# Performance work log

Measured on AMD Instinct MI355X. Metric: run time of the kernel, lower is better.

Reference implementation:

```python
import jax, jax.numpy as jnp
import numpy as np

BLOCK = 8
ITERS = 8
EPS = 1e-5
SHAPE = (64, 64, 64)
BATCH = 16


def overlapping_blocks(x, bs):
    # x: [B, M, N, K] -> per-block copies with a 1-cell zero-padded halo:
    # [B, nm, nn, nk, bs+2, bs+2, bs+2]
    B, M, N, K = x.shape
    p = jnp.pad(x, ((0, 0), (1, 1), (1, 1), (1, 1)))

    def gather(a, axis, n, size):
        idx = (jnp.arange(n)[:, None] * bs + jnp.arange(size)[None, :]).reshape(-1)
        a = jnp.take(a, idx, axis=axis)
        return a.reshape(a.shape[:axis] + (n, size) + a.shape[axis + 1:])

    nm, nn, nk = M // bs, N // bs, K // bs
    p = gather(p, 1, nm, bs + 2)   # [B, nm, P, N+2, K+2]
    p = gather(p, 3, nn, bs + 2)   # [B, nm, P, nn, P, K+2]
    p = gather(p, 5, nk, bs + 2)   # [B, nm, P, nn, P, nk, P]
    return p.transpose(0, 1, 3, 5, 2, 4, 6)


def param_blocks(w, bs):
    # [..., M, N, K] -> [..., nm, nn, nk, bs, bs, bs] (non-overlapping)
    lead = w.shape[:-3]
    M, N, K = w.shape[-3:]
    w = w.reshape(*lead, M // bs, bs, N // bs, bs, K // bs, bs)
    nl = len(lead)
    perm = tuple(range(nl)) + (nl, nl + 2, nl + 4, nl + 1, nl + 3, nl + 5)
    return w.transpose(perm)


def gridnet_step(weight, bias, residual_scale, x, inner_iterations, block_size,
                 eps=EPS, normalize=True):
    bs = block_size
    blocks = overlapping_blocks(x, bs)            # [B, nm, nn, nk, P, P, P]
    wb = param_blocks(weight, bs)                 # [27, nm, nn, nk, bs, bs, bs]
    bb = param_blocks(bias, bs)                   # [nm, nn, nk, bs, bs, bs]
    rb = param_blocks(residual_scale, bs)
    inner = (slice(None),) * 4 + (slice(1, -1),) * 3

    for _ in range(inner_iterations):
        if normalize:
            mean = blocks.mean(axis=(-3, -2, -1), keepdims=True)
            var = blocks.var(axis=(-3, -2, -1), keepdims=True)
            normed = (blocks - mean) / jnp.sqrt(var + eps)
        else:
            normed = blocks
        dot = jnp.zeros_like(blocks[inner])
        tap = 0
        for dx in range(3):
            for dy in range(3):
                for dz in range(3):
                    nb = normed[..., dx:dx + bs, dy:dy + bs, dz:dz + bs]
                    dot = dot + nb * wb[tap]
                    tap += 1
        out = blocks[inner] + rb * jax.nn.silu(dot + bb)
        # only interior cells update; halo stays at initial (synced) values
        blocks = blocks.at[inner].set(out)

    y = blocks[inner]                              # [B, nm, nn, nk, bs, bs, bs]
    B, nm, nn, nk = y.shape[:4]
    return y.transpose(0, 1, 4, 2, 5, 3, 6).reshape(B, nm * bs, nn * bs, nk * bs)


def setup_inputs() -> dict:
    key = jax.random.key(0)
    k_w, k_x = jax.random.split(key)
    M, N, K = SHAPE
    weight = jax.random.normal(k_w, (27, M, N, K), dtype=jnp.float32) / np.sqrt(27.0).astype(np.float32)
    bias = jnp.zeros((M, N, K), dtype=jnp.float32)
    residual_scale = jnp.ones((M, N, K), dtype=jnp.float32)
    x = jax.random.normal(k_x, (BATCH, M, N, K), dtype=jnp.float32)
    return {"weight": weight, "bias": bias, "residual_scale": residual_scale, "x": x}


def reference(weight, bias, residual_scale, x):
    return gridnet_step(weight, bias, residual_scale, x, ITERS, BLOCK, EPS, True)
```

## Files before the change

kernel.cpp:

```cpp
#include <hip/hip_runtime.h>

typedef _Float16 h2 __attribute__((ext_vector_type(2)));
typedef _Float16 h8 __attribute__((ext_vector_type(8)));

#define WSTRIDE 108

template <int CTRL>
__device__ __forceinline__ float dpp_stage(float v) {
    int x = __builtin_amdgcn_update_dpp(0, __float_as_int(v), CTRL, 0xf, 0xf, true);
    return v + __int_as_float(x);
}
__device__ __forceinline__ float wave_sum(float v) {
    v = dpp_stage<0x111>(v);
    v = dpp_stage<0x112>(v);
    v = dpp_stage<0x114>(v);
    v = dpp_stage<0x118>(v);
    v = dpp_stage<0x142>(v);
    v = dpp_stage<0x143>(v);
    return v;
}
__device__ __forceinline__ float bcast63(float v) {
    return __int_as_float(__builtin_amdgcn_readlane(__float_as_int(v), 63));
}
__device__ __forceinline__ h2 mid2(h2 lo, h2 hi) {
    int r = __builtin_amdgcn_alignbit(__builtin_bit_cast(int, hi),
                                      __builtin_bit_cast(int, lo), 16);
    return __builtin_bit_cast(h2, r);
}
__device__ __forceinline__ h2 pkrtz(float a, float b) {
    return __builtin_bit_cast(h2, __builtin_amdgcn_cvt_pkrtz(a, b));
}

#define MEMFENCE() asm volatile("" ::: "memory")

#define SL(W, K) __builtin_shufflevector(W, W, 2*(K), 2*(K)+1)

#define COLT(O, T) {                                                           \
    h8 WA = wp8[(T)];                                                          \
    h8 WB = wp8[(T) + 1];                                                      \
    h8 WC = wp8[(T) + 2];                                                      \
    h2 D0 = bp[(O) + 0], D1 = bp[(O) + 1], D2 = bp[(O) + 2],                   \
       D3 = bp[(O) + 3], D4 = bp[(O) + 4];                                     \
    h2 M0 = mid2(D0, D1), M1 = mid2(D1, D2), M2 = mid2(D2, D3),                \
       M3 = mid2(D3, D4);                                                      \
    dd0 = __builtin_elementwise_fma(D0, SL(WA, 0), dd0);                       \
    dd1 = __builtin_elementwise_fma(D1, SL(WA, 1), dd1);                       \
    dd2 = __builtin_elementwise_fma(D2, SL(WA, 2), dd2);                       \
    dd3 = __builtin_elementwise_fma(D3, SL(WA, 3), dd3);                       \
    dd0 = __builtin_elementwise_fma(M0, SL(WB, 0), dd0);                       \
    dd1 = __builtin_elementwise_fma(M1, SL(WB, 1), dd1);                       \
    dd2 = __builtin_elementwise_fma(M2, SL(WB, 2), dd2);                       \
    dd3 = __builtin_elementwise_fma(M3, SL(WB, 3), dd3);                       \
    dd0 = __builtin_elementwise_fma(D1, SL(WC, 0), dd0);                       \
    dd1 = __builtin_elementwise_fma(D2, SL(WC, 1), dd1);                       \
    dd2 = __builtin_elementwise_fma(D3, SL(WC, 2), dd2);                       \
    dd3 = __builtin_elementwise_fma(D4, SL(WC, 3), dd3); }

#define OUTK(CK, DDF, SWK, BK, RK) {                                           \
    float u = fmaf(fmaf(SWK, nmean, DDF), istd, BK);                           \
    CK += RK * (u * __builtin_amdgcn_rcpf(1.f + __expf(-u))); }

__global__ __launch_bounds__(512, 1)
void gridnet_kernel(const float* __restrict__ W,
                    const float* __restrict__ Bias,
                    const float* __restrict__ Rs,
                    const float* __restrict__ X,
                    float* __restrict__ Y,
                    int n_batch)
{
    __shared__ __align__(16) int wlds[64 * WSTRIDE];
    __shared__ __align__(16) h2 dbuf[8][500];

    const int tid  = threadIdx.x;
    const int wave = tid >> 6;
    const int lane = tid & 63;
    const int lx   = lane >> 3;
    const int ly   = lane & 7;

    const int no    = n_batch >> 3;
    const int bid   = (int)blockIdx.x;
    const int r     = bid / no;
    const int ob    = bid - r * no;
    const int batch = 8 * ob + wave;
    const int gm0 = (r >> 6) << 3;
    const int gn0 = ((r >> 3) & 7) << 3;
    const int gk0 = (r & 7) << 3;

    const float* xb = X + ((size_t)batch << 18);
    h2* const my = dbuf[wave];

    float s_all = 0.f, q_all = 0.f, s_int = 0.f, q_int = 0.f;
    #pragma unroll 1
    for (int c = lane; c < 100; c += 64) {
        int x = c / 10, y = c - (c / 10) * 10;
        int m = gm0 + x - 1, n = gn0 + y - 1;
        bool row_ok = ((unsigned)m < 64u) & ((unsigned)n < 64u);
        float4 fa = {0.f, 0.f, 0.f, 0.f}, fb = {0.f, 0.f, 0.f, 0.f};
        float vz0 = 0.f, vz9 = 0.f;
        if (row_ok) {
            const float* rp = xb + (m * 4096 + n * 64);
            fa = *(const float4*)(rp + gk0);
            fb = *(const float4*)(rp + gk0 + 4);
            if (gk0 > 0)  vz0 = rp[gk0 - 1];
            if (gk0 < 56) vz9 = rp[gk0 + 8];
        }
        h2 d0 = pkrtz(vz0, fa.x), d1 = pkrtz(fa.y, fa.z), d2 = pkrtz(fa.w, fb.x),
           d3 = pkrtz(fb.y, fb.z), d4 = pkrtz(fb.w, vz9);
        my[c * 5 + 0] = d0; my[c * 5 + 1] = d1; my[c * 5 + 2] = d2;
        my[c * 5 + 3] = d3; my[c * 5 + 4] = d4;
        float t0 = (float)d0.x, t1 = (float)d0.y, t2 = (float)d1.x,
              t3 = (float)d1.y, t4 = (float)d2.x, t5 = (float)d2.y,
              t6 = (float)d3.x, t7 = (float)d3.y, t8 = (float)d4.x,
              t9 = (float)d4.y;
        float s8 = t1 + t2 + t3 + t4 + t5 + t6 + t7 + t8;
        float q8 = t1*t1 + t2*t2 + t3*t3 + t4*t4 + t5*t5 + t6*t6 + t7*t7 + t8*t8;
        s_all += s8 + t0 + t9;
        q_all += q8 + t0*t0 + t9*t9;
        bool inter = ((unsigned)(x - 1) < 8u) & ((unsigned)(y - 1) < 8u);
        if (inter) { s_int += s8; q_int += q8; }
    }

    #pragma unroll 1
    for (int j = tid; j < 1728; j += 512) {
        int tap = j >> 6;
        int pos = j & 63;
        int plx = pos >> 3, ply = pos & 7;
        const float* wp = W + ((size_t)tap << 18)
                        + (((size_t)(gm0 + plx)) << 12) + ((gn0 + ply) << 6) + gk0;
        float4 fa = *(const float4*)(wp);
        float4 fb = *(const float4*)(wp + 4);
        int4 v = { __builtin_bit_cast(int, pkrtz(fa.x, fa.y)),
                   __builtin_bit_cast(int, pkrtz(fa.z, fa.w)),
                   __builtin_bit_cast(int, pkrtz(fb.x, fb.y)),
                   __builtin_bit_cast(int, pkrtz(fb.z, fb.w)) };
        *(int4*)&wlds[pos * WSTRIDE + tap * 4] = v;
    }

    float S_all = bcast63(wave_sum(s_all));
    float Q_all = bcast63(wave_sum(q_all));
    float Si    = bcast63(wave_sum(s_int));
    float Qi    = bcast63(wave_sum(q_int));
    const float halo_s = S_all - Si;
    const float halo_q = Q_all - Qi;

    __syncthreads();

    const h8* const wp8 = (const h8*)&wlds[lane * WSTRIDE];
    h2* const bp = &my[5 * (lx * 10 + ly)];

    float sw0=0.f, sw1=0.f, sw2=0.f, sw3=0.f, sw4=0.f, sw5=0.f, sw6=0.f, sw7=0.f;
    #pragma unroll
    for (int t = 0; t < 27; ++t) {
        h8 w = wp8[t];
        sw0 += (float)w[0]; sw1 += (float)w[1]; sw2 += (float)w[2];
        sw3 += (float)w[3]; sw4 += (float)w[4]; sw5 += (float)w[5];
        sw6 += (float)w[6]; sw7 += (float)w[7];
    }

    const size_t ofs = (((size_t)(gm0 + lx)) << 12) + ((gn0 + ly) << 6) + gk0;
    float4 ba = *(const float4*)(Bias + ofs), bb = *(const float4*)(Bias + ofs + 4);
    float4 ra = *(const float4*)(Rs + ofs),   rb = *(const float4*)(Rs + ofs + 4);

    h2 e0 = bp[55], e1 = bp[56], e2 = bp[57], e3 = bp[58], e4 = bp[59];
    float z0f = (float)e0.x, z9f = (float)e4.y;
    float c1 = (float)e0.y, c2 = (float)e1.x, c3 = (float)e1.y, c4 = (float)e2.x,
          c5 = (float)e2.y, c6 = (float)e3.x, c7 = (float)e3.y, c8 = (float)e4.x;

    const float inv_n = 1.0f / 1000.0f;

    #pragma unroll 1
    for (int it = 0; it < 8; ++it) {
        float mean  = (halo_s + Si) * inv_n;
        float qmean = (halo_q + Qi) * inv_n;
        float istd  = rsqrtf(qmean - mean * mean + 1e-5f);
        float nmean = -mean;

        h2 dd0 = { (_Float16)0.f, (_Float16)0.f };
        h2 dd1 = dd0, dd2 = dd0, dd3 = dd0;
        COLT(0,    0)
        COLT(5,    3)
        COLT(10,   6)
        COLT(50,   9)
        COLT(55,  12)
        COLT(60,  15)
        COLT(100, 18)
        COLT(105, 21)
        COLT(110, 24)

        MEMFENCE();

        OUTK(c1, (float)dd0.x, sw0, ba.x, ra.x)
        OUTK(c2, (float)dd0.y, sw1, ba.y, ra.y)
        OUTK(c3, (float)dd1.x, sw2, ba.z, ra.z)
        OUTK(c4, (float)dd1.y, sw3, ba.w, ra.w)
        OUTK(c5, (float)dd2.x, sw4, bb.x, rb.x)
        OUTK(c6, (float)dd2.y, sw5, bb.y, rb.y)
        OUTK(c7, (float)dd3.x, sw6, bb.z, rb.z)
        OUTK(c8, (float)dd3.y, sw7, bb.w, rb.w)

        if (it != 7) {
            e0 = pkrtz(z0f, c1); e1 = pkrtz(c2, c3); e2 = pkrtz(c4, c5);
            e3 = pkrtz(c6, c7); e4 = pkrtz(c8, z9f);
            bp[55] = e0; bp[56] = e1; bp[57] = e2; bp[58] = e3; bp[59] = e4;

            MEMFENCE();

            float sp = ((c1 + c2) + (c3 + c4)) + ((c5 + c6) + (c7 + c8));
            float qp = ((c1*c1 + c2*c2) + (c3*c3 + c4*c4)) +
                       ((c5*c5 + c6*c6) + (c7*c7 + c8*c8));
            Si = bcast63(wave_sum(sp));
            Qi = bcast63(wave_sum(qp));
        }
    }

    float* yp = Y + ((size_t)batch << 18) + ofs;
    *(float4*)(yp)     = make_float4(c1, c2, c3, c4);
    *(float4*)(yp + 4) = make_float4(c5, c6, c7, c8);
}

extern "C" void kernel_launch(void* const* d_in, const int* in_sizes, int n_in,
                              void* d_out, int out_size, void* d_ws, size_t ws_size,
                              hipStream_t stream) {
    const float* W = (const float*)d_in[0];
    const float* B = (const float*)d_in[1];
    const float* R = (const float*)d_in[2];
    const float* X = (const float*)d_in[3];
    float* Y = (float*)d_out;

    int n_batch = in_sizes[3] >> 18;
    dim3 grid(512 * (n_batch >> 3)), block(512);
    hipLaunchKernelGGL(gridnet_kernel, grid, block, 0, stream, W, B, R, X, Y, n_batch);
}
```

Baseline: 147.0 us.

## Process two batch elements per wave to reuse stencil weights from registers

Each wave now handles two batch samples, so the block shrinks from 8 waves to 4 while still covering 8 samples. Every weight vector read from LDS feeds the FMAs of both samples, which halves weight LDS traffic per output and gives more independent FMA chains for instruction-level parallelism. The cost is roughly doubled register pressure and fewer waves per block, which can cut latency hiding and occupancy.

```diff
diff --git a/kernel.cpp b/kernel.cpp
--- a/kernel.cpp
+++ b/kernel.cpp
@@ -35,32 +35,48 @@
 
 #define SL(W, K) __builtin_shufflevector(W, W, 2*(K), 2*(K)+1)
 
-#define COLT(O, T) {                                                           \
+#define COLT2(O, T) {                                                          \
     h8 WA = wp8[(T)];                                                          \
     h8 WB = wp8[(T) + 1];                                                      \
     h8 WC = wp8[(T) + 2];                                                      \
-    h2 D0 = bp[(O) + 0], D1 = bp[(O) + 1], D2 = bp[(O) + 2],                   \
-       D3 = bp[(O) + 3], D4 = bp[(O) + 4];                                     \
-    h2 M0 = mid2(D0, D1), M1 = mid2(D1, D2), M2 = mid2(D2, D3),                \
-       M3 = mid2(D3, D4);                                                      \
-    dd0 = __builtin_elementwise_fma(D0, SL(WA, 0), dd0);                       \
-    dd1 = __builtin_elementwise_fma(D1, SL(WA, 1), dd1);                       \
-    dd2 = __builtin_elementwise_fma(D2, SL(WA, 2), dd2);                       \
-    dd3 = __builtin_elementwise_fma(D3, SL(WA, 3), dd3);                       \
-    dd0 = __builtin_elementwise_fma(M0, SL(WB, 0), dd0);                       \
-    dd1 = __builtin_elementwise_fma(M1, SL(WB, 1), dd1);                       \
-    dd2 = __builtin_elementwise_fma(M2, SL(WB, 2), dd2);                       \
-    dd3 = __builtin_elementwise_fma(M3, SL(WB, 3), dd3);                       \
-    dd0 = __builtin_elementwise_fma(D1, SL(WC, 0), dd0);                       \
-    dd1 = __builtin_elementwise_fma(D2, SL(WC, 1), dd1);                       \
-    dd2 = __builtin_elementwise_fma(D3, SL(WC, 2), dd2);                       \
-    dd3 = __builtin_elementwise_fma(D4, SL(WC, 3), dd3); }
-
-#define OUTK(CK, DDF, SWK, BK, RK) {                                           \
-    float u = fmaf(fmaf(SWK, nmean, DDF), istd, BK);                           \
+    h2 A0 = bpA[(O) + 0], A1 = bpA[(O) + 1], A2 = bpA[(O) + 2],                \
+       A3 = bpA[(O) + 3], A4 = bpA[(O) + 4];                                   \
+    h2 MA0 = mid2(A0, A1), MA1 = mid2(A1, A2), MA2 = mid2(A2, A3),             \
+       MA3 = mid2(A3, A4);                                                     \
+    h2 B0 = bpB[(O) + 0], B1 = bpB[(O) + 1], B2 = bpB[(O) + 2],                \
+       B3 = bpB[(O) + 3], B4 = bpB[(O) + 4];                                   \
+    h2 MB0 = mid2(B0, B1), MB1 = mid2(B1, B2), MB2 = mid2(B2, B3),             \
+       MB3 = mid2(B3, B4);                                                     \
+    ddA0 = __builtin_elementwise_fma(A0, SL(WA, 0), ddA0);                     \
+    ddA1 = __builtin_elementwise_fma(A1, SL(WA, 1), ddA1);                     \
+    ddA2 = __builtin_elementwise_fma(A2, SL(WA, 2), ddA2);                     \
+    ddA3 = __builtin_elementwise_fma(A3, SL(WA, 3), ddA3);                     \
+    ddB0 = __builtin_elementwise_fma(B0, SL(WA, 0), ddB0);                     \
+    ddB1 = __builtin_elementwise_fma(B1, SL(WA, 1), ddB1);                     \
+    ddB2 = __builtin_elementwise_fma(B2, SL(WA, 2), ddB2);                     \
+    ddB3 = __builtin_elementwise_fma(B3, SL(WA, 3), ddB3);                     \
+    ddA0 = __builtin_elementwise_fma(MA0, SL(WB, 0), ddA0);                    \
+    ddA1 = __builtin_elementwise_fma(MA1, SL(WB, 1), ddA1);                    \
+    ddA2 = __builtin_elementwise_fma(MA2, SL(WB, 2), ddA2);                    \
+    ddA3 = __builtin_elementwise_fma(MA3, SL(WB, 3), ddA3);                    \
+    ddB0 = __builtin_elementwise_fma(MB0, SL(WB, 0), ddB0);                    \
+    ddB1 = __builtin_elementwise_fma(MB1, SL(WB, 1), ddB1);                    \
+    ddB2 = __builtin_elementwise_fma(MB2, SL(WB, 2), ddB2);                    \
+    ddB3 = __builtin_elementwise_fma(MB3, SL(WB, 3), ddB3);                    \
+    ddA0 = __builtin_elementwise_fma(A1, SL(WC, 0), ddA0);                     \
+    ddA1 = __builtin_elementwise_fma(A2, SL(WC, 1), ddA1);                     \
+    ddA2 = __builtin_elementwise_fma(A3, SL(WC, 2), ddA2);                     \
+    ddA3 = __builtin_elementwise_fma(A4, SL(WC, 3), ddA3);                     \
+    ddB0 = __builtin_elementwise_fma(B1, SL(WC, 0), ddB0);                     \
+    ddB1 = __builtin_elementwise_fma(B2, SL(WC, 1), ddB1);                     \
+    ddB2 = __builtin_elementwise_fma(B3, SL(WC, 2), ddB2);                     \
+    ddB3 = __builtin_elementwise_fma(B4, SL(WC, 3), ddB3); }
+
+#define OUTK(CK, DDF, SWK, BK, RK, NM, IS) {                                   \
+    float u = fmaf(fmaf(SWK, NM, DDF), IS, BK);                                \
     CK += RK * (u * __builtin_amdgcn_rcpf(1.f + __expf(-u))); }
 
-__global__ __launch_bounds__(512, 1)
+__global__ __launch_bounds__(256, 1)
 void gridnet_kernel(const float* __restrict__ W,
                     const float* __restrict__ Bias,
                     const float* __restrict__ Rs,
@@ -81,47 +97,64 @@
     const int bid   = (int)blockIdx.x;
     const int r     = bid / no;
     const int ob    = bid - r * no;
-    const int batch = 8 * ob + wave;
+    const int batchA = 8 * ob + 2 * wave;
     const int gm0 = (r >> 6) << 3;
     const int gn0 = ((r >> 3) & 7) << 3;
     const int gk0 = (r & 7) << 3;
 
-    const float* xb = X + ((size_t)batch << 18);
-    h2* const my = dbuf[wave];
-
-    float s_all = 0.f, q_all = 0.f, s_int = 0.f, q_int = 0.f;
+    const float* xb = X + ((size_t)batchA << 18);
+    h2* const myA = dbuf[2 * wave];
+    h2* const myB = dbuf[2 * wave + 1];
+
+    float sA_all = 0.f, qA_all = 0.f, sA_int = 0.f, qA_int = 0.f;
+    float sB_all = 0.f, qB_all = 0.f, sB_int = 0.f, qB_int = 0.f;
     #pragma unroll 1
     for (int c = lane; c < 100; c += 64) {
         int x = c / 10, y = c - (c / 10) * 10;
         int m = gm0 + x - 1, n = gn0 + y - 1;
         bool row_ok = ((unsigned)m < 64u) & ((unsigned)n < 64u);
         float4 fa = {0.f, 0.f, 0.f, 0.f}, fb = {0.f, 0.f, 0.f, 0.f};
-        float vz0 = 0.f, vz9 = 0.f;
+        float4 ga = {0.f, 0.f, 0.f, 0.f}, gb = {0.f, 0.f, 0.f, 0.f};
+        float vz0A = 0.f, vz9A = 0.f, vz0B = 0.f, vz9B = 0.f;
         if (row_ok) {
             const float* rp = xb + (m * 4096 + n * 64);
+            const float* rq = rp + (1 << 18);
             fa = *(const float4*)(rp + gk0);
             fb = *(const float4*)(rp + gk0 + 4);
-            if (gk0 > 0)  vz0 = rp[gk0 - 1];
-            if (gk0 < 56) vz9 = rp[gk0 + 8];
+            ga = *(const float4*)(rq + gk0);
+            gb = *(const float4*)(rq + gk0 + 4);
+            if (gk0 > 0)  { vz0A = rp[gk0 - 1]; vz0B = rq[gk0 - 1]; }
+            if (gk0 < 56) { vz9A = rp[gk0 + 8]; vz9B = rq[gk0 + 8]; }
         }
-        h2 d0 = pkrtz(vz0, fa.x), d1 = pkrtz(fa.y, fa.z), d2 = pkrtz(fa.w, fb.x),
-           d3 = pkrtz(fb.y, fb.z), d4 = pkrtz(fb.w, vz9);
-        my[c * 5 + 0] = d0; my[c * 5 + 1] = d1; my[c * 5 + 2] = d2;
-        my[c * 5 + 3] = d3; my[c * 5 + 4] = d4;
-        float t0 = (float)d0.x, t1 = (float)d0.y, t2 = (float)d1.x,
-              t3 = (float)d1.y, t4 = (float)d2.x, t5 = (float)d2.y,
-              t6 = (float)d3.x, t7 = (float)d3.y, t8 = (float)d4.x,
-              t9 = (float)d4.y;
-        float s8 = t1 + t2 + t3 + t4 + t5 + t6 + t7 + t8;
-        float q8 = t1*t1 + t2*t2 + t3*t3 + t4*t4 + t5*t5 + t6*t6 + t7*t7 + t8*t8;
-        s_all += s8 + t0 + t9;
-        q_all += q8 + t0*t0 + t9*t9;
+        h2 a0 = pkrtz(vz0A, fa.x), a1 = pkrtz(fa.y, fa.z), a2 = pkrtz(fa.w, fb.x),
+           a3 = pkrtz(fb.y, fb.z), a4 = pkrtz(fb.w, vz9A);
+        h2 b0 = pkrtz(vz0B, ga.x), b1 = pkrtz(ga.y, ga.z), b2 = pkrtz(ga.w, gb.x),
+           b3 = pkrtz(gb.y, gb.z), b4 = pkrtz(gb.w, vz9B);
+        myA[c * 5 + 0] = a0; myA[c * 5 + 1] = a1; myA[c * 5 + 2] = a2;
+        myA[c * 5 + 3] = a3; myA[c * 5 + 4] = a4;
+        myB[c * 5 + 0] = b0; myB[c * 5 + 1] = b1; myB[c * 5 + 2] = b2;
+        myB[c * 5 + 3] = b3; myB[c * 5 + 4] = b4;
+        float tA0=(float)a0.x, tA1=(float)a0.y, tA2=(float)a1.x, tA3=(float)a1.y,
+              tA4=(float)a2.x, tA5=(float)a2.y, tA6=(float)a3.x, tA7=(float)a3.y,
+              tA8=(float)a4.x, tA9=(float)a4.y;
+        float tB0=(float)b0.x, tB1=(float)b0.y, tB2=(float)b1.x, tB3=(float)b1.y,
+              tB4=(float)b2.x, tB5=(float)b2.y, tB6=(float)b3.x, tB7=(float)b3.y,
+              tB8=(float)b4.x, tB9=(float)b4.y;
+        float sA8 = tA1+tA2+tA3+tA4+tA5+tA6+tA7+tA8;
+        float qA8 = tA1*tA1+tA2*tA2+tA3*tA3+tA4*tA4+tA5*tA5+tA6*tA6+tA7*tA7+tA8*tA8;
+        float sB8 = tB1+tB2+tB3+tB4+tB5+tB6+tB7+tB8;
+        float qB8 = tB1*tB1+tB2*tB2+tB3*tB3+tB4*tB4+tB5*tB5+tB6*tB6+tB7*tB7+tB8*tB8;
+        sA_all += sA8 + tA0 + tA9;
+        qA_all += qA8 + tA0*tA0 + tA9*tA9;
+        sB_all += sB8 + tB0 + tB9;
+        qB_all += qB8 + tB0*tB0 + tB9*tB9;
         bool inter = ((unsigned)(x - 1) < 8u) & ((unsigned)(y - 1) < 8u);
-        if (inter) { s_int += s8; q_int += q8; }
+        if (inter) { sA_int += sA8; qA_int += qA8;
+                     sB_int += sB8; qB_int += qB8; }
     }
 
     #pragma unroll 1
-    for (int j = tid; j < 1728; j += 512) {
+    for (int j = tid; j < 1728; j += 256) {
         int tap = j >> 6;
         int pos = j & 63;
         int plx = pos >> 3, ply = pos & 7;
@@ -136,17 +169,22 @@
         *(int4*)&wlds[pos * WSTRIDE + tap * 4] = v;
     }
 
-    float S_all = bcast63(wave_sum(s_all));
-    float Q_all = bcast63(wave_sum(q_all));
-    float Si    = bcast63(wave_sum(s_int));
-    float Qi    = bcast63(wave_sum(q_int));
-    const float halo_s = S_all - Si;
-    const float halo_q = Q_all - Qi;
+    float SA_all = bcast63(wave_sum(sA_all));
+    float QA_all = bcast63(wave_sum(qA_all));
+    float SiA    = bcast63(wave_sum(sA_int));
+    float QiA    = bcast63(wave_sum(qA_int));
+    float SB_all = bcast63(wave_sum(sB_all));
+    float QB_all = bcast63(wave_sum(qB_all));
+    float SiB    = bcast63(wave_sum(sB_int));
+    float QiB    = bcast63(wave_sum(qB_int));
+    const float halo_sA = SA_all - SiA, halo_qA = QA_all - QiA;
+    const float halo_sB = SB_all - SiB, halo_qB = QB_all - QiB;
 
     __syncthreads();
 
     const h8* const wp8 = (const h8*)&wlds[lane * WSTRIDE];
-    h2* const bp = &my[5 * (lx * 10 + ly)];
+    h2* const bpA = &myA[5 * (lx * 10 + ly)];
+    h2* const bpB = &myB[5 * (lx * 10 + ly)];
 
     float sw0=0.f, sw1=0.f, sw2=0.f, sw3=0.f, sw4=0.f, sw5=0.f, sw6=0.f, sw7=0.f;
     #pragma unroll
@@ -161,61 +199,87 @@
     float4 ba = *(const float4*)(Bias + ofs), bb = *(const float4*)(Bias + ofs + 4);
     float4 ra = *(const float4*)(Rs + ofs),   rb = *(const float4*)(Rs + ofs + 4);
 
-    h2 e0 = bp[55], e1 = bp[56], e2 = bp[57], e3 = bp[58], e4 = bp[59];
-    float z0f = (float)e0.x, z9f = (float)e4.y;
-    float c1 = (float)e0.y, c2 = (float)e1.x, c3 = (float)e1.y, c4 = (float)e2.x,
-          c5 = (float)e2.y, c6 = (float)e3.x, c7 = (float)e3.y, c8 = (float)e4.x;
+    h2 eA0 = bpA[55], eA1 = bpA[56], eA2 = bpA[57], eA3 = bpA[58], eA4 = bpA[59];
+    h2 eB0 = bpB[55], eB1 = bpB[56], eB2 = bpB[57], eB3 = bpB[58], eB4 = bpB[59];
+    float z0A = (float)eA0.x, z9A = (float)eA4.y;
+    float z0B = (float)eB0.x, z9B = (float)eB4.y;
+    float cA1=(float)eA0.y, cA2=(float)eA1.x, cA3=(float)eA1.y, cA4=(float)eA2.x,
+          cA5=(float)eA2.y, cA6=(float)eA3.x, cA7=(float)eA3.y, cA8=(float)eA4.x;
+    float cB1=(float)eB0.y, cB2=(float)eB1.x, cB3=(float)eB1.y, cB4=(float)eB2.x,
+          cB5=(float)eB2.y, cB6=(float)eB3.x, cB7=(float)eB3.y, cB8=(float)eB4.x;
 
     const float inv_n = 1.0f / 1000.0f;
 
     #pragma unroll 1
     for (int it = 0; it < 8; ++it) {
-        float mean  = (halo_s + Si) * inv_n;
-        float qmean = (halo_q + Qi) * inv_n;
-        float istd  = rsqrtf(qmean - mean * mean + 1e-5f);
-        float nmean = -mean;
-
-        h2 dd0 = { (_Float16)0.f, (_Float16)0.f };
-        h2 dd1 = dd0, dd2 = dd0, dd3 = dd0;
-        COLT(0,    0)
-        COLT(5,    3)
-        COLT(10,   6)
-        COLT(50,   9)
-        COLT(55,  12)
-        COLT(60,  15)
-        COLT(100, 18)
-        COLT(105, 21)
-        COLT(110, 24)
+        float meanA  = (halo_sA + SiA) * inv_n;
+        float istdA  = rsqrtf((halo_qA + QiA) * inv_n - meanA * meanA + 1e-5f);
+        float nmeanA = -meanA;
+        float meanB  = (halo_sB + SiB) * inv_n;
+        float istdB  = rsqrtf((halo_qB + QiB) * inv_n - meanB * meanB + 1e-5f);
+        float nmeanB = -meanB;
+
+        h2 ddA0 = { (_Float16)0.f, (_Float16)0.f };
+        h2 ddA1 = ddA0, ddA2 = ddA0, ddA3 = ddA0;
+        h2 ddB0 = ddA0, ddB1 = ddA0, ddB2 = ddA0, ddB3 = ddA0;
+        COLT2(0,    0)
+        COLT2(5,    3)
+        COLT2(10,   6)
+        COLT2(50,   9)
+        COLT2(55,  12)
+        COLT2(60,  15)
+        COLT2(100, 18)
+        COLT2(105, 21)
+        COLT2(110, 24)
 
         MEMFENCE();
 
-        OUTK(c1, (float)dd0.x, sw0, ba.x, ra.x)
-        OUTK(c2, (float)dd0.y, sw1, ba.y, ra.y)
-        OUTK(c3, (float)dd1.x, sw2, ba.z, ra.z)
-        OUTK(c4, (float)dd1.y, sw3, ba.w, ra.w)
-        OUTK(c5, (float)dd2.x, sw4, bb.x, rb.x)
-        OUTK(c6, (float)dd2.y, sw5, bb.y, rb.y)
-        OUTK(c7, (float)dd3.x, sw6, bb.z, rb.z)
-        OUTK(c8, (float)dd3.y, sw7, bb.w, rb.w)
+        OUTK(cA1, (float)ddA0.x, sw0, ba.x, ra.x, nmeanA, istdA)
+        OUTK(cA2, (float)ddA0.y, sw1, ba.y, ra.y, nmeanA, istdA)
+        OUTK(cA3, (float)ddA1.x, sw2, ba.z, ra.z, nmeanA, istdA)
+        OUTK(cA4, (float)ddA1.y, sw3, ba.w, ra.w, nmeanA, istdA)
+        OUTK(cA5, (float)ddA2.x, sw4, bb.x, rb.x, nmeanA, istdA)
+        OUTK(cA6, (float)ddA2.y, sw5, bb.y, rb.y, nmeanA, istdA)
+        OUTK(cA7, (float)ddA3.x, sw6, bb.z, rb.z, nmeanA, istdA)
+        OUTK(cA8, (float)ddA3.y, sw7, bb.w, rb.w, nmeanA, istdA)
+        OUTK(cB1, (float)ddB0.x, sw0, ba.x, ra.x, nmeanB, istdB)
+        OUTK(cB2, (float)ddB0.y, sw1, ba.y, ra.y, nmeanB, istdB)
+        OUTK(cB3, (float)ddB1.x, sw2, ba.z, ra.z, nmeanB, istdB)
+        OUTK(cB4, (float)ddB1.y, sw3, ba.w, ra.w, nmeanB, istdB)
+        OUTK(cB5, (float)ddB2.x, sw4, bb.x, rb.x, nmeanB, istdB)
+        OUTK(cB6, (float)ddB2.y, sw5, bb.y, rb.y, nmeanB, istdB)
+        OUTK(cB7, (float)ddB3.x, sw6, bb.z, rb.z, nmeanB, istdB)
+        OUTK(cB8, (float)ddB3.y, sw7, bb.w, rb.w, nmeanB, istdB)
 
         if (it != 7) {
-            e0 = pkrtz(z0f, c1); e1 = pkrtz(c2, c3); e2 = pkrtz(c4, c5);
-            e3 = pkrtz(c6, c7); e4 = pkrtz(c8, z9f);
-            bp[55] = e0; bp[56] = e1; bp[57] = e2; bp[58] = e3; bp[59] = e4;
+            eA0 = pkrtz(z0A, cA1); eA1 = pkrtz(cA2, cA3); eA2 = pkrtz(cA4, cA5);
+            eA3 = pkrtz(cA6, cA7); eA4 = pkrtz(cA8, z9A);
+            bpA[55] = eA0; bpA[56] = eA1; bpA[57] = eA2; bpA[58] = eA3; bpA[59] = eA4;
+            eB0 = pkrtz(z0B, cB1); eB1 = pkrtz(cB2, cB3); eB2 = pkrtz(cB4, cB5);
+            eB3 = pkrtz(cB6, cB7); eB4 = pkrtz(cB8, z9B);
+            bpB[55] = eB0; bpB[56] = eB1; bpB[57] = eB2; bpB[58] = eB3; bpB[59] = eB4;
 
             MEMFENCE();
 
-            float sp = ((c1 + c2) + (c3 + c4)) + ((c5 + c6) + (c7 + c8));
-            float qp = ((c1*c1 + c2*c2) + (c3*c3 + c4*c4)) +
-                       ((c5*c5 + c6*c6) + (c7*c7 + c8*c8));
-            Si = bcast63(wave_sum(sp));
-            Qi = bcast63(wave_sum(qp));
+            float spA = ((cA1 + cA2) + (cA3 + cA4)) + ((cA5 + cA6) + (cA7 + cA8));
+            float qpA = ((cA1*cA1 + cA2*cA2) + (cA3*cA3 + cA4*cA4)) +
+                        ((cA5*cA5 + cA6*cA6) + (cA7*cA7 + cA8*cA8));
+            float spB = ((cB1 + cB2) + (cB3 + cB4)) + ((cB5 + cB6) + (cB7 + cB8));
+            float qpB = ((cB1*cB1 + cB2*cB2) + (cB3*cB3 + cB4*cB4)) +
+                        ((cB5*cB5 + cB6*cB6) + (cB7*cB7 + cB8*cB8));
+            SiA = bcast63(wave_sum(spA));
+            QiA = bcast63(wave_sum(qpA));
+            SiB = bcast63(wave_sum(spB));
+            QiB = bcast63(wave_sum(qpB));
         }
     }
 
-    float* yp = Y + ((size_t)batch << 18) + ofs;
-    *(float4*)(yp)     = make_float4(c1, c2, c3, c4);
-    *(float4*)(yp + 4) = make_float4(c5, c6, c7, c8);
+    float* yp = Y + ((size_t)batchA << 18) + ofs;
+    *(float4*)(yp)     = make_float4(cA1, cA2, cA3, cA4);
+    *(float4*)(yp + 4) = make_float4(cA5, cA6, cA7, cA8);
+    float* yq = yp + (1 << 18);
+    *(float4*)(yq)     = make_float4(cB1, cB2, cB3, cB4);
+    *(float4*)(yq + 4) = make_float4(cB5, cB6, cB7, cB8);
 }
 
 extern "C" void kernel_launch(void* const* d_in, const int* in_sizes, int n_in,
@@ -228,6 +292,6 @@
     float* Y = (float*)d_out;
 
     int n_batch = in_sizes[3] >> 18;
-    dim3 grid(512 * (n_batch >> 3)), block(512);
+    dim3 grid(512 * (n_batch >> 3)), block(256);
     hipLaunchKernelGGL(gridnet_kernel, grid, block, 0, stream, W, B, R, X, Y, n_batch);
 }
```

Result: slower. 154.7 us (+5.2%).
